# Optimization experiments

Measured on AMD Instinct MI355X. Metric: run time of the kernel, lower is better.

The kernel has to match this reference:

```python
import jax, jax.numpy as jnp
import numpy as np

C = 128
EPS = 1e-5


def _ln(x, g, b):
    m = jnp.mean(x, axis=-1, keepdims=True)
    v = jnp.mean((x - m) ** 2, axis=-1, keepdims=True)
    return (x - m) * jax.lax.rsqrt(v + EPS) * g + b


def setup_inputs() -> dict:
    key = jax.random.key(0)
    ks = jax.random.split(key, 10)
    B, N = 1, 384
    s = 1.0 / np.sqrt(C)
    inp = {
        "z": jax.random.normal(ks[0], (B, N, N, C), dtype=jnp.float32),
        "ln1_g": jnp.ones((C,), jnp.float32),
        "ln1_b": jnp.zeros((C,), jnp.float32),
        "ln2_g": jnp.ones((C,), jnp.float32),
        "ln2_b": jnp.zeros((C,), jnp.float32),
        "Wa": jax.random.uniform(ks[1], (C, C), jnp.float32, -s, s),
        "ba": jnp.zeros((C,), jnp.float32),
        "Wga": jax.random.uniform(ks[2], (C, C), jnp.float32, -s, s),
        "bga": jnp.zeros((C,), jnp.float32),
        "Wb": jax.random.uniform(ks[3], (C, C), jnp.float32, -s, s),
        "bb": jnp.zeros((C,), jnp.float32),
        "Wgb": jax.random.uniform(ks[4], (C, C), jnp.float32, -s, s),
        "bgb": jnp.zeros((C,), jnp.float32),
        "Wg": jax.random.uniform(ks[5], (C, C), jnp.float32, -s, s),
        "bg": jnp.zeros((C,), jnp.float32),
        "Wo": jax.random.uniform(ks[6], (C, C), jnp.float32, -s, s),
        "bo": jnp.zeros((C,), jnp.float32),
    }
    return inp


def reference(z, ln1_g, ln1_b, ln2_g, ln2_b, Wa, ba, Wga, bga, Wb, bb, Wgb, bgb, Wg, bg, Wo, bo):
    # z: (B, i, j, c)
    zn = _ln(z, ln1_g, ln1_b)
    a = (zn @ Wa + ba) * jax.nn.sigmoid(zn @ Wga + bga)      # (B,i,k,c)
    b = (zn @ Wb + bb) * jax.nn.sigmoid(zn @ Wgb + bgb)      # (B,j,k,c)
    gate = jax.nn.sigmoid(zn @ Wg + bg)                      # (B,i,j,c)
    o = jnp.einsum('bikc,bjkc->bijc', a, b)                  # outgoing triangle update
    return gate * (_ln(o, ln2_g, ln2_b) @ Wo + bo)
```

## Files before the change

### kernel.cpp

```cpp
#include <hip/hip_runtime.h>
#include <hip/hip_bf16.h>
#include <stdint.h>

typedef __bf16 bf16x8 __attribute__((ext_vector_type(8)));
typedef float floatx4 __attribute__((ext_vector_type(4)));

#define RR 147456
#define NC 128
#define NN 384

union U32B { unsigned int u; __bf16 h[2]; };

__device__ inline floatx4 zero4() { floatx4 v; v[0]=0.f; v[1]=0.f; v[2]=0.f; v[3]=0.f; return v; }
__device__ inline float sigmoidf_(float x) { return 1.f / (1.f + __expf(-x)); }

__global__ __launch_bounds__(256) void k0_wt(
    const float* __restrict__ w0, const float* __restrict__ w1,
    const float* __restrict__ w2, const float* __restrict__ w3,
    const float* __restrict__ w4, const float* __restrict__ w5,
    __bf16* __restrict__ wt)
{
  const float* w;
  switch (blockIdx.x) {
    case 0: w = w0; break; case 1: w = w1; break; case 2: w = w2; break;
    case 3: w = w3; break; case 4: w = w4; break; default: w = w5; break;
  }
  __bf16* out = wt + blockIdx.x * 16384;
  const int t = threadIdx.x;
  for (int it = 0; it < 64; ++it) {
    int f = it * 256 + t;
    int n = f >> 7, k = f & 127;
    out[f] = (__bf16)w[k * 128 + n];
  }
}

__global__ __launch_bounds__(256) void k2_ln_gemm(
    const float* __restrict__ z, const float* __restrict__ ln1g, const float* __restrict__ ln1b,
    const __bf16* __restrict__ wt,
    const float* __restrict__ ba, const float* __restrict__ bga,
    const float* __restrict__ bb, const float* __restrict__ bgb,
    const float* __restrict__ bg,
    __bf16* __restrict__ at, __bf16* __restrict__ bt, __bf16* __restrict__ gate)
{
  __shared__ __align__(16) __bf16 zns[64][136];
  __shared__ __align__(16) __bf16 wts[128][136];
  const int t = threadIdx.x;
  const int w = t >> 6, lane = t & 63;
  const int l15 = lane & 15, quad = lane >> 4;
  const int r0 = blockIdx.x * 64;

  {
    float gg0 = ln1g[2*lane], gg1 = ln1g[2*lane+1];
    float bb0 = ln1b[2*lane], bb1 = ln1b[2*lane+1];
    for (int rr = 0; rr < 16; ++rr) {
      int row = w * 16 + rr;
      float2 xz = *(const float2*)(z + (size_t)(r0 + row) * NC + 2*lane);
      float x0 = xz.x, x1 = xz.y;
      float s = x0 + x1, q = x0*x0 + x1*x1;
      #pragma unroll
      for (int m = 1; m < 64; m <<= 1) { s += __shfl_xor(s, m); q += __shfl_xor(q, m); }
      float mean = s * (1.f/128.f);
      float var  = q * (1.f/128.f) - mean*mean;
      float rs = rsqrtf(var + 1e-5f);
      U32B uo;
      uo.h[0] = (__bf16)((x0 - mean) * rs * gg0 + bb0);
      uo.h[1] = (__bf16)((x1 - mean) * rs * gg1 + bb1);
      *(unsigned int*)&zns[row][2*lane] = uo.u;
    }
  }
  __syncthreads();

  auto stage = [&](const __bf16* wsrc) {
    #pragma unroll
    for (int it = 0; it < 8; ++it) {
      int f = (it * 256 + t) * 8;
      int n = f >> 7, k = f & 127;
      *(uint4*)&wts[n][k] = *(const uint4*)(wsrc + f);
    }
  };
  auto gemm = [&](floatx4* acc) {
    #pragma unroll
    for (int nt = 0; nt < 8; ++nt) acc[nt] = zero4();
    #pragma unroll
    for (int k0 = 0; k0 < 128; k0 += 32) {
      bf16x8 af = *(const bf16x8*)&zns[w*16 + l15][k0 + quad*8];
      #pragma unroll
      for (int nt = 0; nt < 8; ++nt) {
        bf16x8 bfr = *(const bf16x8*)&wts[nt*16 + l15][k0 + quad*8];
        acc[nt] = __builtin_amdgcn_mfma_f32_16x16x32_bf16(af, bfr, acc[nt], 0, 0, 0);
      }
    }
  };
  auto combine_store = [&](const floatx4* aP, const floatx4* aG,
                           const float* bia, const float* big, __bf16* dst) {
    #pragma unroll
    for (int nt = 0; nt < 8; ++nt) {
      int c = nt*16 + l15;
      float bav = bia[c], bgv = big[c];
      union { uint2 u2; __bf16 h[4]; } pk;
      #pragma unroll
      for (int r = 0; r < 4; ++r) {
        float p  = aP[nt][r] + bav;
        float gg = aG[nt][r] + bgv;
        pk.h[r] = (__bf16)(p * sigmoidf_(gg));
      }
      *(uint2*)(dst + (size_t)c * RR + r0 + w*16 + quad*4) = pk.u2;
    }
  };

  floatx4 accP[8], accG[8];

  stage(wt + 0*16384); __syncthreads(); gemm(accP); __syncthreads();
  stage(wt + 1*16384); __syncthreads(); gemm(accG); __syncthreads();
  combine_store(accP, accG, ba, bga, at);
  stage(wt + 2*16384); __syncthreads(); gemm(accP); __syncthreads();
  stage(wt + 3*16384); __syncthreads(); gemm(accG); __syncthreads();
  combine_store(accP, accG, bb, bgb, bt);
  stage(wt + 4*16384); __syncthreads(); gemm(accG); __syncthreads();

  #pragma unroll
  for (int nt = 0; nt < 8; ++nt) {
    int c = nt*16 + l15;
    float bgv = bg[c];
    #pragma unroll
    for (int r = 0; r < 4; ++r)
      zns[w*16 + quad*4 + r][c] = (__bf16)sigmoidf_(accG[nt][r] + bgv);
  }
  __syncthreads();
  {
    int row = t >> 2, c0 = (t & 3) * 32;
    uint4* dst = (uint4*)(gate + (size_t)(r0 + row) * NC + c0);
    const uint4* src = (const uint4*)&zns[row][c0];
    dst[0] = src[0]; dst[1] = src[1]; dst[2] = src[2]; dst[3] = src[3];
  }
}

__global__ __launch_bounds__(256) void k3_tri(
    const __bf16* __restrict__ at, const __bf16* __restrict__ bt, float* __restrict__ o)
{
  __shared__ __align__(16) __bf16 As[128][72];
  __shared__ __align__(16) __bf16 Bs[128][72];
  const int t = threadIdx.x;
  const int w = t >> 6, lane = t & 63, l15 = lane & 15, quad = lane >> 4;
  const int c = blockIdx.y;
  const int i0 = (blockIdx.x / 3) * 128, j0 = (blockIdx.x % 3) * 128;
  const int wi = w >> 1, wj = w & 1;
  const size_t base = (size_t)c * RR;
  const __bf16* A  = at + base;
  const __bf16* Bp = bt + base;

  floatx4 acc[4][4];
  #pragma unroll
  for (int mt = 0; mt < 4; ++mt)
    #pragma unroll
    for (int nt = 0; nt < 4; ++nt) acc[mt][nt] = zero4();

  for (int kk = 0; kk < NN; kk += 64) {
    #pragma unroll
    for (int s2 = 0; s2 < 4; ++s2) {
      int f = s2 * 2048 + t * 8;
      int row = f >> 6, k = f & 63;
      *(uint4*)&As[row][k] = *(const uint4*)(A  + (size_t)(i0 + row) * NN + kk + k);
      *(uint4*)&Bs[row][k] = *(const uint4*)(Bp + (size_t)(j0 + row) * NN + kk + k);
    }
    __syncthreads();
    #pragma unroll
    for (int k0 = 0; k0 < 64; k0 += 32) {
      bf16x8 af[4], bfr[4];
      #pragma unroll
      for (int mt = 0; mt < 4; ++mt) af[mt]  = *(const bf16x8*)&As[wi*64 + mt*16 + l15][k0 + quad*8];
      #pragma unroll
      for (int nt = 0; nt < 4; ++nt) bfr[nt] = *(const bf16x8*)&Bs[wj*64 + nt*16 + l15][k0 + quad*8];
      #pragma unroll
      for (int mt = 0; mt < 4; ++mt)
        #pragma unroll
        for (int nt = 0; nt < 4; ++nt)
          acc[mt][nt] = __builtin_amdgcn_mfma_f32_16x16x32_bf16(af[mt], bfr[nt], acc[mt][nt], 0, 0, 0);
    }
    __syncthreads();
  }
  #pragma unroll
  for (int mt = 0; mt < 4; ++mt) {
    #pragma unroll
    for (int r = 0; r < 4; ++r) {
      int i = i0 + wi*64 + mt*16 + quad*4 + r;
      float* orow = o + base + (size_t)i * NN + j0 + wj*64;
      #pragma unroll
      for (int nt = 0; nt < 4; ++nt) orow[nt*16 + l15] = acc[mt][nt][r];
    }
  }
}

__global__ __launch_bounds__(256) void k4_out(
    const float* __restrict__ o, const __bf16* __restrict__ gate,
    const float* __restrict__ ln2g, const float* __restrict__ ln2b,
    const __bf16* __restrict__ wot, const float* __restrict__ bo,
    float* __restrict__ out)
{
  __shared__ __align__(16) float  osb[64][129];
  __shared__ __align__(16) __bf16 ans[64][136];
  __shared__ __align__(16) __bf16 wts[128][136];
  __shared__ __align__(16) __bf16 gbf[64][136];
  const int t = threadIdx.x;
  const int w = t >> 6, lane = t & 63, l15 = lane & 15, quad = lane >> 4;
  const int r0 = blockIdx.x * 64;

  #pragma unroll
  for (int it = 0; it < 8; ++it) {
    int f = it * 1024 + t * 4;
    int cx = f >> 6, p = f & 63;
    float4 v = *(const float4*)(o + (size_t)cx * RR + r0 + p);
    osb[p+0][cx] = v.x; osb[p+1][cx] = v.y; osb[p+2][cx] = v.z; osb[p+3][cx] = v.w;
  }
  {
    int row = t >> 2, c0 = (t & 3) * 32;
    const uint4* src = (const uint4*)(gate + (size_t)(r0 + row) * NC + c0);
    uint4* dst = (uint4*)&gbf[row][c0];
    dst[0] = src[0]; dst[1] = src[1]; dst[2] = src[2]; dst[3] = src[3];
  }
  #pragma unroll
  for (int it = 0; it < 8; ++it) {
    int f = (it * 256 + t) * 8;
    int n = f >> 7, k = f & 127;
    *(uint4*)&wts[n][k] = *(const uint4*)(wot + f);
  }
  __syncthreads();

  {
    float gg0 = ln2g[2*lane], gg1 = ln2g[2*lane+1];
    float bb0 = ln2b[2*lane], bb1 = ln2b[2*lane+1];
    for (int rr = 0; rr < 16; ++rr) {
      int row = w * 16 + rr;
      float x0 = osb[row][2*lane], x1 = osb[row][2*lane+1];
      float s = x0 + x1, q = x0*x0 + x1*x1;
      #pragma unroll
      for (int m = 1; m < 64; m <<= 1) { s += __shfl_xor(s, m); q += __shfl_xor(q, m); }
      float mean = s * (1.f/128.f);
      float var  = q * (1.f/128.f) - mean*mean;
      float rs = rsqrtf(var + 1e-5f);
      U32B uo;
      uo.h[0] = (__bf16)((x0 - mean) * rs * gg0 + bb0);
      uo.h[1] = (__bf16)((x1 - mean) * rs * gg1 + bb1);
      *(unsigned int*)&ans[row][2*lane] = uo.u;
    }
  }
  __syncthreads();

  floatx4 acc[8];
  #pragma unroll
  for (int nt = 0; nt < 8; ++nt) acc[nt] = zero4();
  #pragma unroll
  for (int k0 = 0; k0 < 128; k0 += 32) {
    bf16x8 af = *(const bf16x8*)&ans[w*16 + l15][k0 + quad*8];
    #pragma unroll
    for (int nt = 0; nt < 8; ++nt) {
      bf16x8 bfr = *(const bf16x8*)&wts[nt*16 + l15][k0 + quad*8];
      acc[nt] = __builtin_amdgcn_mfma_f32_16x16x32_bf16(af, bfr, acc[nt], 0, 0, 0);
    }
  }

  #pragma unroll
  for (int nt = 0; nt < 8; ++nt) {
    int c = nt*16 + l15;
    float bov = bo[c];
    #pragma unroll
    for (int r = 0; r < 4; ++r) {
      int rl = w*16 + quad*4 + r;
      out[(size_t)(r0 + rl) * NC + c] = (float)gbf[rl][c] * (acc[nt][r] + bov);
    }
  }
}

extern "C" void kernel_launch(void* const* d_in, const int* in_sizes, int n_in,
                              void* d_out, int out_size, void* d_ws, size_t ws_size,
                              hipStream_t stream) {
  const float* z    = (const float*)d_in[0];
  const float* l1g  = (const float*)d_in[1];
  const float* l1b  = (const float*)d_in[2];
  const float* l2g  = (const float*)d_in[3];
  const float* l2b  = (const float*)d_in[4];
  const float* Wa   = (const float*)d_in[5];
  const float* ba   = (const float*)d_in[6];
  const float* Wga  = (const float*)d_in[7];
  const float* bga  = (const float*)d_in[8];
  const float* Wb   = (const float*)d_in[9];
  const float* bb   = (const float*)d_in[10];
  const float* Wgb  = (const float*)d_in[11];
  const float* bgb  = (const float*)d_in[12];
  const float* Wg   = (const float*)d_in[13];
  const float* bg   = (const float*)d_in[14];
  const float* Wo   = (const float*)d_in[15];
  const float* bo   = (const float*)d_in[16];

  char* ws = (char*)d_ws;
  __bf16* at_  = (__bf16*)(ws + 0);
  __bf16* bt_  = (__bf16*)(ws + 37748736);
  __bf16* gate = (__bf16*)(ws + 75497472);
  float*  o    = (float*) (ws + 113246208);
  __bf16* wt   = (__bf16*)(ws + 188743680);

  hipLaunchKernelGGL(k0_wt, dim3(6), dim3(256), 0, stream, Wa, Wga, Wb, Wgb, Wg, Wo, wt);
  hipLaunchKernelGGL(k2_ln_gemm, dim3(2304), dim3(256), 0, stream,
                     z, l1g, l1b, wt, ba, bga, bb, bgb, bg, at_, bt_, gate);
  hipLaunchKernelGGL(k3_tri, dim3(9, 128), dim3(256), 0, stream, at_, bt_, o);
  hipLaunchKernelGGL(k4_out, dim3(2304), dim3(256), 0, stream,
                     o, gate, l2g, l2b, wt + 5*16384, bo, (float*)d_out);
}
```

Baseline: 339.5 us.

## Double rows per block in LN+projection kernel to reuse staged weights

The fused layernorm and projection kernel now handles 128 rows per block instead of 64. Each wave computes two 16-row M tiles, so every weight fragment loaded from shared memory feeds two MFMAs, and each staged weight matrix is amortized over twice as many rows. The grid is halved to 1152 blocks. It also drops the barrier between the last GEMM and the gate writeback into zns. The trade-off is twice the accumulator registers and more shared memory per block, which may lower occupancy.

```diff
diff --git a/kernel.cpp b/kernel.cpp
--- a/kernel.cpp
+++ b/kernel.cpp
@@ -42,18 +42,18 @@
     const float* __restrict__ bg,
     __bf16* __restrict__ at, __bf16* __restrict__ bt, __bf16* __restrict__ gate)
 {
-  __shared__ __align__(16) __bf16 zns[64][136];
+  __shared__ __align__(16) __bf16 zns[128][136];
   __shared__ __align__(16) __bf16 wts[128][136];
   const int t = threadIdx.x;
   const int w = t >> 6, lane = t & 63;
   const int l15 = lane & 15, quad = lane >> 4;
-  const int r0 = blockIdx.x * 64;
+  const int r0 = blockIdx.x * 128;
 
   {
     float gg0 = ln1g[2*lane], gg1 = ln1g[2*lane+1];
     float bb0 = ln1b[2*lane], bb1 = ln1b[2*lane+1];
-    for (int rr = 0; rr < 16; ++rr) {
-      int row = w * 16 + rr;
+    for (int rr = 0; rr < 32; ++rr) {
+      int row = w * 32 + rr;
       float2 xz = *(const float2*)(z + (size_t)(r0 + row) * NC + 2*lane);
       float x0 = xz.x, x1 = xz.y;
       float s = x0 + x1, q = x0*x0 + x1*x1;
@@ -78,37 +78,47 @@
       *(uint4*)&wts[n][k] = *(const uint4*)(wsrc + f);
     }
   };
-  auto gemm = [&](floatx4* acc) {
-    #pragma unroll
-    for (int nt = 0; nt < 8; ++nt) acc[nt] = zero4();
+  auto gemm = [&](floatx4 (*acc)[8]) {
+    #pragma unroll
+    for (int mt = 0; mt < 2; ++mt)
+      #pragma unroll
+      for (int nt = 0; nt < 8; ++nt) acc[mt][nt] = zero4();
     #pragma unroll
     for (int k0 = 0; k0 < 128; k0 += 32) {
-      bf16x8 af = *(const bf16x8*)&zns[w*16 + l15][k0 + quad*8];
+      bf16x8 af[2];
+      #pragma unroll
+      for (int mt = 0; mt < 2; ++mt)
+        af[mt] = *(const bf16x8*)&zns[w*32 + mt*16 + l15][k0 + quad*8];
       #pragma unroll
       for (int nt = 0; nt < 8; ++nt) {
         bf16x8 bfr = *(const bf16x8*)&wts[nt*16 + l15][k0 + quad*8];
-        acc[nt] = __builtin_amdgcn_mfma_f32_16x16x32_bf16(af, bfr, acc[nt], 0, 0, 0);
+        #pragma unroll
+        for (int mt = 0; mt < 2; ++mt)
+          acc[mt][nt] = __builtin_amdgcn_mfma_f32_16x16x32_bf16(af[mt], bfr, acc[mt][nt], 0, 0, 0);
       }
     }
   };
-  auto combine_store = [&](const floatx4* aP, const floatx4* aG,
+  auto combine_store = [&](floatx4 (*aP)[8], floatx4 (*aG)[8],
                            const float* bia, const float* big, __bf16* dst) {
     #pragma unroll
-    for (int nt = 0; nt < 8; ++nt) {
-      int c = nt*16 + l15;
-      float bav = bia[c], bgv = big[c];
-      union { uint2 u2; __bf16 h[4]; } pk;
-      #pragma unroll
-      for (int r = 0; r < 4; ++r) {
-        float p  = aP[nt][r] + bav;
-        float gg = aG[nt][r] + bgv;
-        pk.h[r] = (__bf16)(p * sigmoidf_(gg));
+    for (int mt = 0; mt < 2; ++mt) {
+      #pragma unroll
+      for (int nt = 0; nt < 8; ++nt) {
+        int c = nt*16 + l15;
+        float bav = bia[c], bgv = big[c];
+        union { uint2 u2; __bf16 h[4]; } pk;
+        #pragma unroll
+        for (int r = 0; r < 4; ++r) {
+          float p  = aP[mt][nt][r] + bav;
+          float gg = aG[mt][nt][r] + bgv;
+          pk.h[r] = (__bf16)(p * sigmoidf_(gg));
+        }
+        *(uint2*)(dst + (size_t)c * RR + r0 + w*32 + mt*16 + quad*4) = pk.u2;
       }
-      *(uint2*)(dst + (size_t)c * RR + r0 + w*16 + quad*4) = pk.u2;
     }
   };
 
-  floatx4 accP[8], accG[8];
+  floatx4 accP[2][8], accG[2][8];
 
   stage(wt + 0*16384); __syncthreads(); gemm(accP); __syncthreads();
   stage(wt + 1*16384); __syncthreads(); gemm(accG); __syncthreads();
@@ -116,19 +126,23 @@
   stage(wt + 2*16384); __syncthreads(); gemm(accP); __syncthreads();
   stage(wt + 3*16384); __syncthreads(); gemm(accG); __syncthreads();
   combine_store(accP, accG, bb, bgb, bt);
-  stage(wt + 4*16384); __syncthreads(); gemm(accG); __syncthreads();
-
-  #pragma unroll
-  for (int nt = 0; nt < 8; ++nt) {
-    int c = nt*16 + l15;
-    float bgv = bg[c];
-    #pragma unroll
-    for (int r = 0; r < 4; ++r)
-      zns[w*16 + quad*4 + r][c] = (__bf16)sigmoidf_(accG[nt][r] + bgv);
+  stage(wt + 4*16384); __syncthreads(); gemm(accG);
+
+  #pragma unroll
+  for (int mt = 0; mt < 2; ++mt) {
+    #pragma unroll
+    for (int nt = 0; nt < 8; ++nt) {
+      int c = nt*16 + l15;
+      float bgv = bg[c];
+      #pragma unroll
+      for (int r = 0; r < 4; ++r)
+        zns[w*32 + mt*16 + quad*4 + r][c] = (__bf16)sigmoidf_(accG[mt][nt][r] + bgv);
+    }
   }
   __syncthreads();
-  {
-    int row = t >> 2, c0 = (t & 3) * 32;
+  #pragma unroll
+  for (int half = 0; half < 2; ++half) {
+    int row = half*64 + (t >> 2), c0 = (t & 3) * 32;
     uint4* dst = (uint4*)(gate + (size_t)(r0 + row) * NC + c0);
     const uint4* src = (const uint4*)&zns[row][c0];
     dst[0] = src[0]; dst[1] = src[1]; dst[2] = src[2]; dst[3] = src[3];
@@ -300,7 +314,7 @@
   __bf16* wt   = (__bf16*)(ws + 188743680);
 
   hipLaunchKernelGGL(k0_wt, dim3(6), dim3(256), 0, stream, Wa, Wga, Wb, Wgb, Wg, Wo, wt);
-  hipLaunchKernelGGL(k2_ln_gemm, dim3(2304), dim3(256), 0, stream,
+  hipLaunchKernelGGL(k2_ln_gemm, dim3(1152), dim3(256), 0, stream,
                      z, l1g, l1b, wt, ba, bga, bb, bgb, bg, at_, bt_, gate);
   hipLaunchKernelGGL(k3_tri, dim3(9, 128), dim3(256), 0, stream, at_, bt_, o);
   hipLaunchKernelGGL(k4_out, dim3(2304), dim3(256), 0, stream,
```

After: 393.5 us. +15.9%, slower.

## Split LN into its own kernel and make projection GEMM weight-stationary

Applied to the files above, without the earlier changes.

Layer norm is split out into a kernel that writes normalized bf16 rows to the workspace, reusing the buffer that later holds o. The projection GEMM becomes a persistent, weight-stationary kernel with a grid of 288 by 3. Each block loads its one or two weight matrices into XOR-swizzled shared memory once and reuses them across 8 row tiles, which removes the repeated per-tile restaging of all five weights and the syncs between stages. In exchange it adds an extra bf16 round trip of zn through global memory, reads each zn tile three times, and uses about 80KB of LDS per block, which limits occupancy.

```diff
diff --git a/kernel.cpp b/kernel.cpp
--- a/kernel.cpp
+++ b/kernel.cpp
@@ -8,6 +8,7 @@
 #define RR 147456
 #define NC 128
 #define NN 384
+#define T_TILES 8
 
 union U32B { unsigned int u; __bf16 h[2]; };
 
@@ -34,104 +35,126 @@
   }
 }
 
-__global__ __launch_bounds__(256) void k2_ln_gemm(
-    const float* __restrict__ z, const float* __restrict__ ln1g, const float* __restrict__ ln1b,
-    const __bf16* __restrict__ wt,
+__global__ __launch_bounds__(256) void k2a_ln(
+    const float* __restrict__ z, const float* __restrict__ ln1g,
+    const float* __restrict__ ln1b, __bf16* __restrict__ zn)
+{
+  const int t = threadIdx.x;
+  const int w = t >> 6, lane = t & 63;
+  const int r0 = blockIdx.x * 64;
+  float gg0 = ln1g[2*lane], gg1 = ln1g[2*lane+1];
+  float bb0 = ln1b[2*lane], bb1 = ln1b[2*lane+1];
+  for (int rr = 0; rr < 16; ++rr) {
+    int row = w * 16 + rr;
+    float2 xz = *(const float2*)(z + (size_t)(r0 + row) * NC + 2*lane);
+    float x0 = xz.x, x1 = xz.y;
+    float s = x0 + x1, q = x0*x0 + x1*x1;
+    #pragma unroll
+    for (int m = 1; m < 64; m <<= 1) { s += __shfl_xor(s, m); q += __shfl_xor(q, m); }
+    float mean = s * (1.f/128.f);
+    float var  = q * (1.f/128.f) - mean*mean;
+    float rs = rsqrtf(var + 1e-5f);
+    U32B uo;
+    uo.h[0] = (__bf16)((x0 - mean) * rs * gg0 + bb0);
+    uo.h[1] = (__bf16)((x1 - mean) * rs * gg1 + bb1);
+    *(unsigned int*)(zn + (size_t)(r0 + row) * NC + 2*lane) = uo.u;
+  }
+}
+
+__global__ __launch_bounds__(256) void k2b_gemm(
+    const __bf16* __restrict__ zn, const __bf16* __restrict__ wt,
     const float* __restrict__ ba, const float* __restrict__ bga,
     const float* __restrict__ bb, const float* __restrict__ bgb,
     const float* __restrict__ bg,
     __bf16* __restrict__ at, __bf16* __restrict__ bt, __bf16* __restrict__ gate)
 {
-  __shared__ __align__(16) __bf16 zns[64][136];
-  __shared__ __align__(16) __bf16 wts[128][136];
+  __shared__ __align__(16) __bf16 zns[64 * 128];
+  __shared__ __align__(16) __bf16 wb0[128 * 128];
+  __shared__ __align__(16) __bf16 wb1[128 * 128];
   const int t = threadIdx.x;
   const int w = t >> 6, lane = t & 63;
   const int l15 = lane & 15, quad = lane >> 4;
-  const int r0 = blockIdx.x * 64;
+  const int v = blockIdx.y;
 
   {
-    float gg0 = ln1g[2*lane], gg1 = ln1g[2*lane+1];
-    float bb0 = ln1b[2*lane], bb1 = ln1b[2*lane+1];
-    for (int rr = 0; rr < 16; ++rr) {
-      int row = w * 16 + rr;
-      float2 xz = *(const float2*)(z + (size_t)(r0 + row) * NC + 2*lane);
-      float x0 = xz.x, x1 = xz.y;
-      float s = x0 + x1, q = x0*x0 + x1*x1;
-      #pragma unroll
-      for (int m = 1; m < 64; m <<= 1) { s += __shfl_xor(s, m); q += __shfl_xor(q, m); }
-      float mean = s * (1.f/128.f);
-      float var  = q * (1.f/128.f) - mean*mean;
-      float rs = rsqrtf(var + 1e-5f);
-      U32B uo;
-      uo.h[0] = (__bf16)((x0 - mean) * rs * gg0 + bb0);
-      uo.h[1] = (__bf16)((x1 - mean) * rs * gg1 + bb1);
-      *(unsigned int*)&zns[row][2*lane] = uo.u;
-    }
-  }
-  __syncthreads();
-
-  auto stage = [&](const __bf16* wsrc) {
+    const __bf16* wg0 = wt + (v == 0 ? 0 : v == 1 ? 2 : 4) * 16384;
+    const __bf16* wg1 = wt + (v == 0 ? 1 : 3) * 16384;
     #pragma unroll
     for (int it = 0; it < 8; ++it) {
-      int f = (it * 256 + t) * 8;
-      int n = f >> 7, k = f & 127;
-      *(uint4*)&wts[n][k] = *(const uint4*)(wsrc + f);
-    }
-  };
-  auto gemm = [&](floatx4* acc) {
+      int c = it * 256 + t;
+      int n = c >> 4, kc = c & 15;
+      int sw = kc ^ (n & 15);
+      *(uint4*)&wb0[n * 128 + sw * 8] = *(const uint4*)(wg0 + c * 8);
+      if (v < 2)
+        *(uint4*)&wb1[n * 128 + sw * 8] = *(const uint4*)(wg1 + c * 8);
+    }
+  }
+
+  auto gemm = [&](const __bf16* wb, floatx4* acc) {
     #pragma unroll
     for (int nt = 0; nt < 8; ++nt) acc[nt] = zero4();
     #pragma unroll
-    for (int k0 = 0; k0 < 128; k0 += 32) {
-      bf16x8 af = *(const bf16x8*)&zns[w*16 + l15][k0 + quad*8];
+    for (int kb = 0; kb < 4; ++kb) {
+      int kc = (kb * 4 + quad) ^ l15;
+      bf16x8 af = *(const bf16x8*)&zns[(w*16 + l15) * 128 + kc * 8];
       #pragma unroll
       for (int nt = 0; nt < 8; ++nt) {
-        bf16x8 bfr = *(const bf16x8*)&wts[nt*16 + l15][k0 + quad*8];
+        bf16x8 bfr = *(const bf16x8*)&wb[(nt*16 + l15) * 128 + kc * 8];
         acc[nt] = __builtin_amdgcn_mfma_f32_16x16x32_bf16(af, bfr, acc[nt], 0, 0, 0);
       }
     }
   };
-  auto combine_store = [&](const floatx4* aP, const floatx4* aG,
-                           const float* bia, const float* big, __bf16* dst) {
-    #pragma unroll
-    for (int nt = 0; nt < 8; ++nt) {
-      int c = nt*16 + l15;
-      float bav = bia[c], bgv = big[c];
-      union { uint2 u2; __bf16 h[4]; } pk;
-      #pragma unroll
-      for (int r = 0; r < 4; ++r) {
-        float p  = aP[nt][r] + bav;
-        float gg = aG[nt][r] + bgv;
-        pk.h[r] = (__bf16)(p * sigmoidf_(gg));
+
+  for (int tile = 0; tile < T_TILES; ++tile) {
+    const int r0 = (blockIdx.x * T_TILES + tile) * 64;
+    __syncthreads();
+    #pragma unroll
+    for (int it = 0; it < 4; ++it) {
+      int c = it * 256 + t;
+      int row = c >> 4, kc = c & 15;
+      int sw = kc ^ (row & 15);
+      *(uint4*)&zns[row * 128 + sw * 8] = *(const uint4*)(zn + (size_t)r0 * NC + c * 8);
+    }
+    __syncthreads();
+
+    if (v < 2) {
+      floatx4 accP[8], accG[8];
+      gemm(wb0, accP);
+      gemm(wb1, accG);
+      const float* biaP = (v == 0) ? ba  : bb;
+      const float* biaG = (v == 0) ? bga : bgb;
+      __bf16* dst = (v == 0) ? at : bt;
+      #pragma unroll
+      for (int nt = 0; nt < 8; ++nt) {
+        int c = nt*16 + l15;
+        float bav = biaP[c], bgv = biaG[c];
+        union { uint2 u2; __bf16 h[4]; } pk;
+        #pragma unroll
+        for (int r = 0; r < 4; ++r) {
+          float p  = accP[nt][r] + bav;
+          float gg = accG[nt][r] + bgv;
+          pk.h[r] = (__bf16)(p * sigmoidf_(gg));
+        }
+        *(uint2*)(dst + (size_t)c * RR + r0 + w*16 + quad*4) = pk.u2;
       }
-      *(uint2*)(dst + (size_t)c * RR + r0 + w*16 + quad*4) = pk.u2;
-    }
-  };
-
-  floatx4 accP[8], accG[8];
-
-  stage(wt + 0*16384); __syncthreads(); gemm(accP); __syncthreads();
-  stage(wt + 1*16384); __syncthreads(); gemm(accG); __syncthreads();
-  combine_store(accP, accG, ba, bga, at);
-  stage(wt + 2*16384); __syncthreads(); gemm(accP); __syncthreads();
-  stage(wt + 3*16384); __syncthreads(); gemm(accG); __syncthreads();
-  combine_store(accP, accG, bb, bgb, bt);
-  stage(wt + 4*16384); __syncthreads(); gemm(accG); __syncthreads();
-
-  #pragma unroll
-  for (int nt = 0; nt < 8; ++nt) {
-    int c = nt*16 + l15;
-    float bgv = bg[c];
-    #pragma unroll
-    for (int r = 0; r < 4; ++r)
-      zns[w*16 + quad*4 + r][c] = (__bf16)sigmoidf_(accG[nt][r] + bgv);
-  }
-  __syncthreads();
-  {
-    int row = t >> 2, c0 = (t & 3) * 32;
-    uint4* dst = (uint4*)(gate + (size_t)(r0 + row) * NC + c0);
-    const uint4* src = (const uint4*)&zns[row][c0];
-    dst[0] = src[0]; dst[1] = src[1]; dst[2] = src[2]; dst[3] = src[3];
+    } else {
+      floatx4 accG[8];
+      gemm(wb0, accG);
+      __bf16* gb = wb1;
+      #pragma unroll
+      for (int nt = 0; nt < 8; ++nt) {
+        int c = nt*16 + l15;
+        float bgv = bg[c];
+        #pragma unroll
+        for (int r = 0; r < 4; ++r)
+          gb[(w*16 + quad*4 + r) * 136 + c] = (__bf16)sigmoidf_(accG[nt][r] + bgv);
+      }
+      __syncthreads();
+      int row = t >> 2, c0 = (t & 3) * 32;
+      uint4* dstg = (uint4*)(gate + (size_t)(r0 + row) * NC + c0);
+      const uint4* src = (const uint4*)&gb[row * 136 + c0];
+      dstg[0] = src[0]; dstg[1] = src[1]; dstg[2] = src[2]; dstg[3] = src[3];
+    }
   }
 }
 
@@ -297,11 +320,13 @@
   __bf16* bt_  = (__bf16*)(ws + 37748736);
   __bf16* gate = (__bf16*)(ws + 75497472);
   float*  o    = (float*) (ws + 113246208);
+  __bf16* zn   = (__bf16*)(ws + 113246208);
   __bf16* wt   = (__bf16*)(ws + 188743680);
 
   hipLaunchKernelGGL(k0_wt, dim3(6), dim3(256), 0, stream, Wa, Wga, Wb, Wgb, Wg, Wo, wt);
-  hipLaunchKernelGGL(k2_ln_gemm, dim3(2304), dim3(256), 0, stream,
-                     z, l1g, l1b, wt, ba, bga, bb, bgb, bg, at_, bt_, gate);
+  hipLaunchKernelGGL(k2a_ln, dim3(2304), dim3(256), 0, stream, z, l1g, l1b, zn);
+  hipLaunchKernelGGL(k2b_gemm, dim3(288, 3), dim3(256), 0, stream,
+                     zn, wt, ba, bga, bb, bgb, bg, at_, bt_, gate);
   hipLaunchKernelGGL(k3_tri, dim3(9, 128), dim3(256), 0, stream, at_, bt_, o);
   hipLaunchKernelGGL(k4_out, dim3(2304), dim3(256), 0, stream,
                      o, gate, l2g, l2b, wt + 5*16384, bo, (float*)d_out);
```

Result: slower. 381.3 us (+12.3%).
